# Kernel tuning notes

Hardware: AMD Instinct MI355X
Metric: run time of the kernel (lower is better)

Reference implementation:

```python
import jax, jax.numpy as jnp
import numpy as np

B, N, DE, H, DH = 2, 1024, 1024, 16, 64
DK = H * DH  # total complex qkv dim per stream
MIN_EXP = -30.0
EPS = 1e-4


def setup_inputs():
    key = jax.random.key(0)
    ks = jax.random.split(key, 8)

    def g(i, shape, sc=1.0):
        return jax.random.normal(ks[i], shape, jnp.float32) * sc

    # RoPE-style per-head frequencies for the conjugate-paired half-dims
    freqs = 10000.0 ** (-np.arange(DH // 2, dtype=np.float64) / (DH // 2))
    omega = jnp.asarray(np.tile(freqs[None, :], (H, 1)), jnp.float32)
    return {
        "x": g(0, (B, N, DE)),
        "Wq": g(1, (DE, 2 * DK), 1.0 / np.sqrt(DE)),
        "Wk": g(2, (DE, 2 * DK), 1.0 / np.sqrt(DE)),
        "Wv": g(3, (DE, 2 * DK), 1.0 / np.sqrt(DE)),
        "Wo": g(4, (2 * DK, DE), 1.0 / np.sqrt(2 * DK)),
        "omega": omega,
        "mu_raw": g(5, (H,)) - 2.0,          # pre-sigmoid decay rates
        "sigma_raw": g(6, (H,)),              # pre-softplus process noise
        "eta_raw": jnp.ones((H,), jnp.float32),
        "gamma_raw": jnp.ones((H,), jnp.float32),
        "tau": jnp.ones((H,), jnp.float32),   # inverse temperature
        "nu_raw": jnp.ones((H,), jnp.float32) * 4.0,  # robustness dof
    }


def reference(x, Wq, Wk, Wv, Wo, omega, mu_raw, sigma_raw, eta_raw, gamma_raw, tau, nu_raw):
    B_, N_, _ = x.shape
    H_, d_half = omega.shape
    DH_ = 2 * d_half
    DKt = H_ * DH_

    def cproj(W):
        z = x @ W                          # [B,N,2D] real/imag packed
        D = W.shape[1] // 2
        zc = jax.lax.complex(z[..., :D], z[..., D:])
        return zc.reshape(B_, N_, H_, DH_)

    q, k, v = cproj(Wq), cproj(Wk), cproj(Wv)

    # complex-conjugate-constrained rotations: omega stacked as [w, -w]
    om = jnp.concatenate([omega, -omega], axis=-1)              # [H,DH]
    t = jnp.arange(N_, dtype=jnp.float32)
    ang = t[:, None, None] * om[None]                           # [N,H,DH]
    phase = jax.lax.complex(jnp.cos(ang), jnp.sin(ang))
    qr = q * phase[None]
    kr = k * phase[None]

    # isotropic SDE decay kernel  E_rel = exp(-mu * |t_i - t_j|)
    mu = jax.nn.sigmoid(mu_raw) + EPS                           # [H]
    dt = jnp.abs(t[:, None] - t[None, :])                       # [N,N]
    E = jnp.exp(jnp.clip(-mu[:, None, None] * dt[None], MIN_EXP, 0.0))  # [H,N,N]

    # Re<q_i, Phi(dt) k_j>  (rotation carried by phases, decay by E)
    s = jnp.einsum('bihd,bjhd->bhij', qr, jnp.conj(kr)).real    # [B,H,N,N]
    qn = (q.real ** 2 + q.imag ** 2).sum(-1).transpose(0, 2, 1)  # [B,H,N]
    kn = (k.real ** 2 + k.imag ** 2).sum(-1).transpose(0, 2, 1)

    # Lyapunov-propagated uncertainty: P(dt) = sigma^2/(2mu)(1 - E^2) + eta^2 + gamma^2
    sigma_sq = jax.nn.softplus(sigma_raw)
    eta_sq = jax.nn.softplus(eta_raw)
    gamma_sq = jax.nn.softplus(gamma_raw)
    V = (sigma_sq / (2.0 * mu))[:, None, None] * (1.0 - E * E) \
        + (eta_sq + gamma_sq)[:, None, None]                    # [H,N,N]

    # per-head Mahalanobis residual under the SDE forecast
    maha = jnp.maximum(qn[..., None] + (E * E)[None] * kn[:, :, None, :]
                       - 2.0 * E[None] * s, 0.0) / V[None]      # [B,H,N,N]

    # robust nu-thresholding (Student-t style) + Gaussian normalization term
    nu = jax.nn.softplus(nu_raw)
    coef = (-0.5 * tau * (nu + DH_))[None, :, None, None]
    logits = coef * jnp.log1p(maha / nu[None, :, None, None]) \
             - 0.5 * DH_ * jnp.log(V)[None]

    causal = (t[:, None] >= t[None, :])
    logits = jnp.where(causal[None, None], logits, -jnp.inf)
    A = jax.nn.softmax(logits, axis=-1)                         # [B,H,N,N]

    out = jnp.einsum('bhij,bjhd->bihd', A.astype(v.dtype), v)   # complex [B,N,H,DH]
    y = jnp.concatenate([out.real.reshape(B_, N_, DKt),
                         out.imag.reshape(B_, N_, DKt)], axis=-1)
    return y @ Wo                                               # [B,N,DE]
```

## Files before the change

### kernel.cpp

```cpp
#include <hip/hip_runtime.h>
#include <math.h>

#define BB      2
#define NN      1024
#define DE_     1024
#define HH      16
#define TWO_DK  2048
#define PK      4194304
#define TBLR    1092

typedef float f32x4  __attribute__((ext_vector_type(4)));
typedef short bf16x8 __attribute__((ext_vector_type(8)));

__device__ __forceinline__ short f2bf(float f) {
    unsigned u = __float_as_uint(f);
    unsigned r = (u + 0x7fffu + ((u >> 16) & 1u)) >> 16;
    return (short)r;
}
__device__ __forceinline__ float bf2f(short v) {
    return __uint_as_float(((unsigned)(unsigned short)v) << 16);
}

__device__ __forceinline__ float fexp2(float x) { return __builtin_amdgcn_exp2f(x); }
__device__ __forceinline__ float flog2(float x) { return __builtin_amdgcn_logf(x); }

#define GLDS16(g, l) __builtin_amdgcn_global_load_lds(                        \
    (const __attribute__((address_space(1))) unsigned int*)(g),               \
    (__attribute__((address_space(3))) unsigned int*)(l), 16, 0, 0)
#define GLDS4(g, l) __builtin_amdgcn_global_load_lds(                         \
    (const __attribute__((address_space(1))) unsigned int*)(g),               \
    (__attribute__((address_space(3))) unsigned int*)(l), 4, 0, 0)

__constant__ int jIT[24] = {7,14,15,15, 6,12,13,13,14, 5,10,11,11,12,
                            4, 8, 9, 9,10, 3, 8, 2, 1, 0};
__constant__ int jJ0[24] = {0, 0, 0, 8, 0, 0, 0, 7, 8, 0, 0, 0, 6, 7,
                            0, 0, 0, 5, 6, 0, 5, 0, 0, 0};
__constant__ int jJ1[24] = {7, 7, 7,15, 6, 6, 6,13,14, 5, 5, 5,11,12,
                            4, 4, 4, 9,10, 3, 8, 2, 1, 0};
__constant__ int jPS[24] = {0, 1, 1, 2, 0, 1, 1, 2, 2, 0, 1, 1, 2, 2,
                            0, 1, 1, 2, 2, 0, 2, 0, 0, 0};

__global__ __launch_bounds__(256) void prep(
    const float* __restrict__ x,
    const float* __restrict__ Wq, const float* __restrict__ Wk,
    const float* __restrict__ Wv, const float* __restrict__ Wo,
    const float* __restrict__ mu_raw, const float* __restrict__ sigma_raw,
    const float* __restrict__ eta_raw, const float* __restrict__ gamma_raw,
    short* __restrict__ xb, short* __restrict__ wt, short* __restrict__ wot,
    float4* __restrict__ tbl) {
    const int z = blockIdx.z;
    if (z == 4) {
        const int flat = blockIdx.y * 32 + blockIdx.x;
        const int i = (flat * 256 + threadIdx.x) * 8;
        float4 v0 = *(const float4*)&x[i];
        float4 v1 = *(const float4*)&x[i + 4];
        short4 o0, o1;
        o0.x = f2bf(v0.x); o0.y = f2bf(v0.y); o0.z = f2bf(v0.z); o0.w = f2bf(v0.w);
        o1.x = f2bf(v1.x); o1.y = f2bf(v1.y); o1.z = f2bf(v1.z); o1.w = f2bf(v1.w);
        *(short4*)&xb[i] = o0; *(short4*)&xb[i + 4] = o1;
        return;
    }
    if (z == 3 && blockIdx.x >= 16) {
        const int idx = blockIdx.y * 16 + (blockIdx.x - 16);
        if (idx >= 80) return;
        const int h = idx / 5, rb = idx % 5;
        const int r = rb * 256 + threadIdx.x;
        if (r >= TBLR) return;
        const float mu = 1.f / (1.f + expf(-mu_raw[h])) + 1e-4f;
        const float Ac = log1pf(expf(sigma_raw[h])) / (2.f * mu);
        const float Cc = log1pf(expf(eta_raw[h])) + log1pf(expf(gamma_raw[h]));
        const float arg = fminf(fmaxf(-mu * (float)(r - 64), -30.f), 0.f);
        const float E   = expf(arg);
        const float V   = fmaf(Ac, 1.f - E * E, Cc);
        tbl[h * TBLR + r] = make_float4(2.f * E, 1.f / V, -32.f * log2f(V), E * E);
        return;
    }
    const float* in; short* out; int R, C;
    if (z < 3) { if (blockIdx.y >= 16) return;
                 in = (z == 0) ? Wq : (z == 1) ? Wk : Wv;
                 out = wt + (size_t)z * 2097152; R = 1024; C = 2048; }
    else       { in = Wo; out = wot; R = 2048; C = 1024; }
    __shared__ float t[64][65];
    const int c0 = blockIdx.x * 64, r0 = blockIdx.y * 64;
    const int tr = threadIdx.x >> 4, tc4 = (threadIdx.x & 15) * 4;
#pragma unroll
    for (int s = 0; s < 4; ++s) {
        const int r = tr + s * 16;
        float4 v = *(const float4*)&in[(size_t)(r0 + r) * C + c0 + tc4];
        t[r][tc4] = v.x; t[r][tc4 + 1] = v.y; t[r][tc4 + 2] = v.z; t[r][tc4 + 3] = v.w;
    }
    __syncthreads();
#pragma unroll
    for (int s = 0; s < 4; ++s) {
        const int oc = tr + s * 16;
        short4 o;
        o.x = f2bf(t[tc4 + 0][oc]); o.y = f2bf(t[tc4 + 1][oc]);
        o.z = f2bf(t[tc4 + 2][oc]); o.w = f2bf(t[tc4 + 3][oc]);
        *(short4*)&out[(size_t)(c0 + oc) * R + r0 + tc4] = o;
    }
}

__global__ __launch_bounds__(256, 5) void gemm_qkv_rot2(
    const short* __restrict__ A, const short* __restrict__ wt,
    const float* __restrict__ omega,
    short* __restrict__ qb, short* __restrict__ kb, short* __restrict__ vtb,
    float* __restrict__ qn_, float* __restrict__ kn_) {
    __shared__ __align__(16) short As[64 * 64];
    __shared__ __align__(16) short Bs[128 * 64];
    __shared__ float sN[4][64];
    const int tid = threadIdx.x;
    const int m0  = blockIdx.x * 64;
    const int h   = blockIdx.y;
    const short* W = wt + (size_t)blockIdx.z * 2097152;

    const short* aP[2]; int aOff[2];
#pragma unroll
    for (int i = 0; i < 2; ++i) {
        const int c   = i * 256 + tid;
        const int row = c >> 3;
        const int src = ((c & 7) ^ (row & 7)) << 3;
        aOff[i] = c * 8;
        aP[i] = A + (size_t)(m0 + row) * 1024 + src;
    }
    const short* bP[4]; int bOff[4];
#pragma unroll
    for (int i = 0; i < 4; ++i) {
        const int c   = i * 256 + tid;
        const int row = c >> 3;
        const int src = ((c & 7) ^ (row & 7)) << 3;
        bOff[i] = c * 8;
        const int t_ = row >> 5, u_ = (row >> 4) & 1, dcol = t_ * 16 + (row & 15);
        bP[i] = W + (size_t)(u_ * 1024 + h * 64 + dcol) * 1024 + src;
    }

    const int lane = tid & 63, w = tid >> 6;
    const int wc = w * 32;
    const int fr = lane & 15;
    const int fo = (lane >> 4) << 3;
    const int sw = (fr & 7) << 3;

    f32x4 acc[4][2];
#pragma unroll
    for (int a = 0; a < 4; ++a)
#pragma unroll
        for (int b = 0; b < 2; ++b) acc[a][b] = (f32x4){0.f, 0.f, 0.f, 0.f};

    for (int k0 = 0; k0 < 1024; k0 += 64) {
#pragma unroll
        for (int i = 0; i < 2; ++i) GLDS16(aP[i] + k0, &As[aOff[i]]);
#pragma unroll
        for (int i = 0; i < 4; ++i) GLDS16(bP[i] + k0, &Bs[bOff[i]]);
        __syncthreads();
#pragma unroll
        for (int ks = 0; ks < 64; ks += 32) {
            bf16x8 af[4], bf[2];
#pragma unroll
            for (int a = 0; a < 4; ++a)
                af[a] = *(const bf16x8*)&As[(a * 16 + fr) * 64 + ((ks + fo) ^ sw)];
#pragma unroll
            for (int b = 0; b < 2; ++b)
                bf[b] = *(const bf16x8*)&Bs[(wc + b * 16 + fr) * 64 + ((ks + fo) ^ sw)];
#pragma unroll
            for (int a = 0; a < 4; ++a)
#pragma unroll
                for (int b = 0; b < 2; ++b)
                    acc[a][b] = __builtin_amdgcn_mfma_f32_16x16x32_bf16(
                        af[a], bf[b], acc[a][b], 0, 0, 0);
        }
        __syncthreads();
    }

    const int quad = lane >> 4, cq = quad * 4, l15 = lane & 15;
    const int bh  = (m0 >> 10) * 16 + h;
    const int nb0 = (m0 & 1023) + cq;

    if (blockIdx.z == 2) {
#pragma unroll
        for (int a = 0; a < 4; ++a) {
#pragma unroll
            for (int b = 0; b < 2; ++b) {
                const int cl = wc + b * 16;
                const int dd = ((cl >> 4) & 1) * 64 + (cl >> 5) * 16 + l15;
                short4 o;
                o.x = f2bf(acc[a][b][0]); o.y = f2bf(acc[a][b][1]);
                o.z = f2bf(acc[a][b][2]); o.w = f2bf(acc[a][b][3]);
                *(short4*)&vtb[((size_t)bh * 128 + dd) * 1024 + nb0 + a * 16] = o;
            }
        }
        return;
    }
    float* nout = (blockIdx.z == 0) ? qn_ : kn_;
    short* obuf = (blockIdx.z == 0) ? qb  : kb;

#pragma unroll
    for (int a = 0; a < 4; ++a) {
        float ns[4] = {0.f, 0.f, 0.f, 0.f};
#pragma unroll
        for (int b = 0; b < 2; ++b)
#pragma unroll
            for (int r = 0; r < 4; ++r)
                ns[r] = fmaf(acc[a][b][r], acc[a][b][r], ns[r]);
#pragma unroll
        for (int m2 = 1; m2 < 16; m2 <<= 1)
#pragma unroll
            for (int r = 0; r < 4; ++r) ns[r] += __shfl_xor(ns[r], m2);
        if (l15 == 0)
#pragma unroll
            for (int r = 0; r < 4; ++r) sN[w][a * 16 + cq + r] = ns[r];
    }
    __syncthreads();
    if (tid < 64)
        nout[(size_t)bh * 1024 + (m0 & 1023) + tid] =
            sN[0][tid] + sN[1][tid] + sN[2][tid] + sN[3][tid];

    {
        const int d = w * 16 + l15;
        const float om = (d < 32) ? omega[h * 32 + d] : -omega[h * 32 + d - 32];
#pragma unroll
        for (int a = 0; a < 4; ++a) {
#pragma unroll
            for (int r = 0; r < 4; ++r) {
                const int n2 = nb0 + a * 16 + r;
                float sn, cs;
                __sincosf((float)n2 * om, &sn, &cs);
                const float re = acc[a][0][r], im = acc[a][1][r];
                short* orow = obuf + ((size_t)bh * 1024 + n2) * 128;
                orow[d]      = f2bf(re * cs - im * sn);
                orow[64 + d] = f2bf(re * sn + im * cs);
            }
        }
    }
}

__global__ __launch_bounds__(256) void attn_mfma(
    const short* __restrict__ qr, const short* __restrict__ kr,
    const short* __restrict__ vt,
    const float* __restrict__ qn, const float* __restrict__ kn,
    const float4* __restrict__ tbl,
    const float* __restrict__ tau_p, const float* __restrict__ nu_raw,
    short* __restrict__ y, short* __restrict__ po0, float* __restrict__ pml) {
    __shared__ __align__(16) short Ks[2][64 * 128];
    __shared__ __align__(16) short Vs[2][128 * 64];
    __shared__ __align__(16) short Ps[64 * 72];
    __shared__ __align__(16) float4 sT[2][128];
    __shared__ float sKn[2][64];

    const int bx   = blockIdx.x;
    const int xcd  = bx & 7;
    const int rest = bx >> 3;
    const int jrk  = rest >> 2;
    const int bh   = xcd * 4 + (rest & 3);
    const int h    = bh & 15;
    const int it   = jIT[jrk];
    const int j0j  = jJ0[jrk];
    const int j1j  = jJ1[jrk];
    const int psel = jPS[jrk];
    const int i0   = it * 64;
    const int pq   = bh * 8 + (it - 8);

    const int tid  = threadIdx.x;
    const int lane = tid & 63, w = tid >> 6;
    const int quad = lane >> 4, l15 = lane & 15;

    const float nu     = log1pf(expf(nu_raw[h]));
    const float coef   = -0.5f * tau_p[h] * (nu + 64.0f);
    const float inv_nu = 1.f / nu;

    const short* Qb  = qr + (size_t)bh * NN * 128;
    const short* Kb  = kr + (size_t)bh * NN * 128;
    const short* Vtb = vt + (size_t)bh * 128 * NN;

#define STAGE(JT, P) do {                                                     \
        const int j0_ = (JT) * 64, dt0_ = i0 - j0_;                           \
        _Pragma("unroll")                                                     \
        for (int i_ = 0; i_ < 4; ++i_) {                                      \
            const int c_ = i_ * 256 + tid, row_ = c_ >> 4;                    \
            const int src_ = ((c_ & 15) ^ (row_ & 7)) * 8;                    \
            GLDS16(Kb + (size_t)(j0_ + row_) * 128 + src_, &Ks[P][c_ * 8]);   \
        }                                                                     \
        _Pragma("unroll")                                                     \
        for (int i_ = 0; i_ < 4; ++i_) {                                      \
            const int c_ = i_ * 256 + tid, d_ = c_ >> 3;                      \
            const int src_ = ((c_ & 7) ^ (d_ & 7)) * 8;                       \
            GLDS16(Vtb + (size_t)d_ * NN + j0_ + src_, &Vs[P][c_ * 8]);       \
        }                                                                     \
        if (w == 0) {                                                         \
            GLDS16(tbl + h * TBLR + 1 + dt0_ + lane, &sT[P][lane]);           \
            GLDS16(tbl + h * TBLR + 65 + dt0_ + lane, &sT[P][64 + lane]);     \
        } else if (w == 1) {                                                  \
            GLDS4(kn + (size_t)bh * NN + j0_ + lane, &sKn[P][lane]);          \
        }                                                                     \
    } while (0)

    bf16x8 qf[4];
    const int arow = i0 + w * 16 + l15;
#pragma unroll
    for (int ks = 0; ks < 4; ++ks)
        qf[ks] = *(const bf16x8*)&Qb[(size_t)arow * 128 + ks * 32 + quad * 8];

    float mrow[4];
    f32x4 o[8];
    f32x4 o9 = (f32x4){0.f, 0.f, 0.f, 0.f};
#pragma unroll
    for (int r = 0; r < 4; ++r) mrow[r] = -INFINITY;
#pragma unroll
    for (int s = 0; s < 8; ++s) o[s] = (f32x4){0.f, 0.f, 0.f, 0.f};
    float qn4[4];
#pragma unroll
    for (int r = 0; r < 4; ++r)
        qn4[r] = qn[(size_t)bh * NN + i0 + w * 16 + quad * 4 + r];

    const bf16x8 onesv = (bf16x8){0x3F80, 0x3F80, 0x3F80, 0x3F80,
                                  0x3F80, 0x3F80, 0x3F80, 0x3F80};

    STAGE(j0j, 0);
    __syncthreads();

    for (int jt = j0j; jt <= j1j; ++jt) {
        const int p = (jt - j0j) & 1;
        if (jt < j1j) STAGE(jt + 1, 1 - p);

        f32x4 sAcc[4];
#pragma unroll
        for (int s = 0; s < 4; ++s) sAcc[s] = (f32x4){0.f, 0.f, 0.f, 0.f};
#pragma unroll
        for (int ks = 0; ks < 4; ++ks) {
#pragma unroll
            for (int s = 0; s < 4; ++s) {
                const int brow = s * 16 + l15;
                bf16x8 bK = *(const bf16x8*)&Ks[p][brow * 128 +
                                                  (((ks * 4 + quad) ^ (brow & 7)) * 8)];
                sAcc[s] = __builtin_amdgcn_mfma_f32_16x16x32_bf16(qf[ks], bK, sAcc[s], 0, 0, 0);
            }
        }

        float al[4];
        bool anyr = false;
#pragma unroll
        for (int r = 0; r < 4; ++r) {
            const int row = w * 16 + quad * 4 + r;
            float lg[4];
#pragma unroll
            for (int s = 0; s < 4; ++s) {
                const int col = s * 16 + l15;
                const float4 T = sT[p][row - col + 63];
                const float sv = sAcc[s][r];
                const float t1 = fmaf(T.w, sKn[p][col], qn4[r]);
                const float maha = fmaxf(fmaf(-T.x, sv, t1), 0.f) * T.y;
                float v = fmaf(coef, flog2(fmaf(maha, inv_nu, 1.f)), T.z);
                if (jt == it && col > row) v = -INFINITY;
                lg[s] = v;
            }
            float mx = fmaxf(fmaxf(lg[0], lg[1]), fmaxf(lg[2], lg[3]));
            mx = fmaxf(mx, __shfl_xor(mx, 1));
            mx = fmaxf(mx, __shfl_xor(mx, 2));
            mx = fmaxf(mx, __shfl_xor(mx, 4));
            mx = fmaxf(mx, __shfl_xor(mx, 8));
            const bool resc = mx > mrow[r] + 16.f;
            const float mu_ = resc ? mx : mrow[r];
            al[r] = resc ? fexp2(mrow[r] - mx) : 1.f;
            mrow[r] = mu_;
            anyr = anyr || resc;
#pragma unroll
            for (int s = 0; s < 4; ++s) {
                const float pv = fexp2(lg[s] - mu_);
                Ps[row * 72 + s * 16 + l15] = f2bf(pv);
            }
        }
        if (anyr) {
#pragma unroll
            for (int s = 0; s < 8; ++s)
#pragma unroll
                for (int r = 0; r < 4; ++r) o[s][r] *= al[r];
#pragma unroll
            for (int r = 0; r < 4; ++r) o9[r] *= al[r];
        }

#pragma unroll
        for (int jc = 0; jc < 2; ++jc) {
            bf16x8 aP = *(const bf16x8*)&Ps[(w * 16 + l15) * 72 + jc * 32 + quad * 8];
#pragma unroll
            for (int sub = 0; sub < 8; ++sub) {
                const int d = sub * 16 + l15;
                bf16x8 bV = *(const bf16x8*)&Vs[p][d * 64 + (((jc * 4 + quad) ^ (d & 7)) * 8)];
                o[sub] = __builtin_amdgcn_mfma_f32_16x16x32_bf16(aP, bV, o[sub], 0, 0, 0);
            }
            o9 = __builtin_amdgcn_mfma_f32_16x16x32_bf16(aP, onesv, o9, 0, 0, 0);
        }
        if (jt < j1j) __syncthreads();
    }
#undef STAGE

    short* dst = (psel == 1) ? po0 : y;
    const size_t rbase = (psel == 1) ? (size_t)pq * 64 : ((size_t)bh * NN + i0);
#pragma unroll
    for (int r = 0; r < 4; ++r) {
        const int lrow = w * 16 + quad * 4 + r;
        const float inv = 1.f / o9[r];
        const size_t base = (rbase + lrow) * 128;
#pragma unroll
        for (int sub = 0; sub < 8; ++sub)
            dst[base + sub * 16 + l15] = f2bf(o[sub][r] * inv);
        if (psel != 0 && l15 == 0)
            pml[(pq * 2 + (psel - 1)) * 64 + lrow] = mrow[r] + flog2(o9[r]);
    }
}

__global__ __launch_bounds__(256) void attn_merge(
    const short* __restrict__ po0, const float* __restrict__ pml,
    short* __restrict__ y) {
    const int qs = blockIdx.x;
    const int bh = qs >> 3, it = (qs & 7) + 8;
    const int t = threadIdx.x;
    const int row = t >> 2, dc = (t & 3) * 32;
    const float m1 = pml[(qs * 2 + 0) * 64 + row];
    const float m2 = pml[(qs * 2 + 1) * 64 + row];
    const float mx = fmaxf(m1, m2);
    const float w1 = fexp2(m1 - mx), w2 = fexp2(m2 - mx);
    const float inv = 1.f / (w1 + w2);
    const float a = w1 * inv, b = w2 * inv;
    const short* s1 = po0 + ((size_t)qs * 64 + row) * 128 + dc;
    short*       s2 = y + ((size_t)bh * NN + it * 64 + row) * 128 + dc;
#pragma unroll
    for (int i = 0; i < 32; i += 8) {
        bf16x8 v1 = *(const bf16x8*)(s1 + i);
        bf16x8 v2 = *(const bf16x8*)(s2 + i);
        bf16x8 ov;
#pragma unroll
        for (int k = 0; k < 8; ++k)
            ov[k] = f2bf(a * bf2f(v1[k]) + b * bf2f(v2[k]));
        *(bf16x8*)(s2 + i) = ov;
    }
}

__global__ __launch_bounds__(256) void gemm_out64(
    const short* __restrict__ yb, const short* __restrict__ wot,
    float* __restrict__ out) {
    __shared__ __align__(16) short As[2][64 * 64];
    __shared__ __align__(16) short Bs[2][64 * 64];
    const int tid = threadIdx.x;
    const int m0  = blockIdx.x * 64;
    const int n0  = blockIdx.y * 64;
    const int bb  = m0 >> 10;

    int aPre[2], aOff[2]; const short* bP[2];
#pragma unroll
    for (int i = 0; i < 2; ++i) {
        const int c = i * 256 + tid, row = c >> 3;
        const int src = ((c & 7) ^ (row & 7)) << 3;
        aPre[i] = ((m0 & 1023) + row) * 128 + src;
        bP[i] = wot + (size_t)(n0 + row) * 2048 + src;
        aOff[i] = c * 8;
    }

    const int lane = tid & 63, w = tid >> 6;
    const int wr = (w >> 1) * 32, wc = (w & 1) * 32;
    const int fr = lane & 15;
    const int fo = (lane >> 4) << 3;
    const int sw = (fr & 7) << 3;

    f32x4 acc[2][2];
#pragma unroll
    for (int a = 0; a < 2; ++a)
#pragma unroll
        for (int b = 0; b < 2; ++b) acc[a][b] = (f32x4){0.f, 0.f, 0.f, 0.f};

#define OSTAGE(KT, P) do {                                                    \
        const int k0_ = (KT) * 64;                                            \
        const int hh_ = (k0_ >> 6) & 15, im_ = k0_ >> 10;                     \
        const short* ab_ = yb + ((size_t)(bb * 16 + hh_) << 17) + im_ * 64;   \
        _Pragma("unroll")                                                     \
        for (int i_ = 0; i_ < 2; ++i_) GLDS16(ab_ + aPre[i_], &As[P][aOff[i_]]); \
        _Pragma("unroll")                                                     \
        for (int i_ = 0; i_ < 2; ++i_) GLDS16(bP[i_] + k0_, &Bs[P][aOff[i_]]);   \
    } while (0)

    OSTAGE(0, 0);
    __syncthreads();

    for (int kt = 0; kt < 32; ++kt) {
        const int p = kt & 1;
        if (kt < 31) OSTAGE(kt + 1, 1 - p);
#pragma unroll
        for (int ks = 0; ks < 64; ks += 32) {
            bf16x8 af[2], bf[2];
#pragma unroll
            for (int a = 0; a < 2; ++a)
                af[a] = *(const bf16x8*)&As[p][(wr + a * 16 + fr) * 64 + ((ks + fo) ^ sw)];
#pragma unroll
            for (int b = 0; b < 2; ++b)
                bf[b] = *(const bf16x8*)&Bs[p][(wc + b * 16 + fr) * 64 + ((ks + fo) ^ sw)];
#pragma unroll
            for (int a = 0; a < 2; ++a)
#pragma unroll
                for (int b = 0; b < 2; ++b)
                    acc[a][b] = __builtin_amdgcn_mfma_f32_16x16x32_bf16(
                        af[a], bf[b], acc[a][b], 0, 0, 0);
        }
        if (kt < 31) __syncthreads();
    }
#undef OSTAGE

    const int cq = (lane >> 4) * 4, l15 = lane & 15;
#pragma unroll
    for (int a = 0; a < 2; ++a)
#pragma unroll
        for (int b = 0; b < 2; ++b)
#pragma unroll
            for (int r = 0; r < 4; ++r)
                out[(size_t)(m0 + wr + a * 16 + cq + r) * 1024 +
                    (n0 + wc + b * 16 + l15)] = acc[a][b][r];
}

extern "C" void kernel_launch(void* const* d_in, const int* in_sizes, int n_in,
                              void* d_out, int out_size, void* d_ws, size_t ws_size,
                              hipStream_t stream) {
    const float* x         = (const float*)d_in[0];
    const float* Wq        = (const float*)d_in[1];
    const float* Wk        = (const float*)d_in[2];
    const float* Wv        = (const float*)d_in[3];
    const float* Wo        = (const float*)d_in[4];
    const float* omega     = (const float*)d_in[5];
    const float* mu_raw    = (const float*)d_in[6];
    const float* sigma_raw = (const float*)d_in[7];
    const float* eta_raw   = (const float*)d_in[8];
    const float* gamma_raw = (const float*)d_in[9];
    const float* tau       = (const float*)d_in[10];
    const float* nu_raw    = (const float*)d_in[11];
    float* out = (float*)d_out;

    short*  qb  = (short*)d_ws;
    short*  kb  = qb + PK;
    short*  vtb = kb + PK;
    float*  qn  = (float*)(vtb + PK);
    float*  kn  = qn + 32768;
    float4* tbl = (float4*)(kn + 32768);
    short*  wot = (short*)(tbl + HH * TBLR);
    short*  wt  = wot + 2097152;
    short*  xb  = wt + 3 * 2097152;
    short*  yb  = wt;
    short*  po0 = wt + 4194304;
    float*  pml = (float*)xb;

    prep<<<dim3(32, 32, 5), 256, 0, stream>>>(
        x, Wq, Wk, Wv, Wo, mu_raw, sigma_raw, eta_raw, gamma_raw,
        xb, wt, wot, tbl);
    gemm_qkv_rot2<<<dim3(32, 16, 3), 256, 0, stream>>>(
        xb, wt, omega, qb, kb, vtb, qn, kn);
    attn_mfma<<<dim3(768), 256, 0, stream>>>(
        qb, kb, vtb, qn, kn, tbl, tau, nu_raw, yb, po0, pml);
    attn_merge<<<dim3(256), 256, 0, stream>>>(po0, pml, yb);
    gemm_out64<<<dim3(32, 16), 256, 0, stream>>>(yb, wot, out);
}
```

Baseline: 200.0 us.

## Rebalance causal attention work into 512 blocks and load QKV weights directly to registers

The causal attention schedule changes from 768 blocks with 24 per-head work units to 512 blocks with 16 groups. Long query tiles are split into two halves that a merge kernel combines, and each short tile is paired with a longer one so the block runs both in turn. This aims for more even per-block work and fewer blocks, at the cost of an extra barrier and a longer serial loop per block. Separately, the QKV GEMM drops the B-matrix LDS staging and loads weight fragments straight from global memory into registers, lowering occupancy bounds from 5 to 4. This saves LDS traffic and space, but the uncoalesced direct global loads may cost more.

After: 217.1 us. 1.09x slower.

```diff
diff --git a/kernel.cpp b/kernel.cpp
--- a/kernel.cpp
+++ b/kernel.cpp
@@ -31,14 +31,11 @@
     (const __attribute__((address_space(1))) unsigned int*)(g),               \
     (__attribute__((address_space(3))) unsigned int*)(l), 4, 0, 0)
 
-__constant__ int jIT[24] = {7,14,15,15, 6,12,13,13,14, 5,10,11,11,12,
-                            4, 8, 9, 9,10, 3, 8, 2, 1, 0};
-__constant__ int jJ0[24] = {0, 0, 0, 8, 0, 0, 0, 7, 8, 0, 0, 0, 6, 7,
-                            0, 0, 0, 5, 6, 0, 5, 0, 0, 0};
-__constant__ int jJ1[24] = {7, 7, 7,15, 6, 6, 6,13,14, 5, 5, 5,11,12,
-                            4, 4, 4, 9,10, 3, 8, 2, 1, 0};
-__constant__ int jPS[24] = {0, 1, 1, 2, 0, 1, 1, 2, 2, 0, 1, 1, 2, 2,
-                            0, 1, 1, 2, 2, 0, 2, 0, 0, 0};
+__constant__ signed char gIT0[16] = {15,15,14,13,12,11,10, 9, 8, 7,14,13,12,11,10, 9};
+__constant__ signed char gJ00[16] = { 0, 8, 0, 0, 0, 0, 0, 0, 0, 0, 8, 8, 8, 8, 8, 8};
+__constant__ signed char gJ10[16] = { 7,15, 7, 7, 7, 7, 7, 7, 8, 7,14,13,12,11,10, 9};
+__constant__ signed char gPS0[16] = { 1, 2, 1, 1, 1, 1, 1, 1, 0, 0, 2, 2, 2, 2, 2, 2};
+__constant__ signed char gIT1[16] = {-1,-1,-1,-1,-1,-1,-1,-1,-1, 0, 1, 2, 3, 4, 5, 6};
 
 __global__ __launch_bounds__(256) void prep(
     const float* __restrict__ x,
@@ -100,13 +97,12 @@
     }
 }
 
-__global__ __launch_bounds__(256, 5) void gemm_qkv_rot2(
+__global__ __launch_bounds__(256, 4) void gemm_qkv_rot2(
     const short* __restrict__ A, const short* __restrict__ wt,
     const float* __restrict__ omega,
     short* __restrict__ qb, short* __restrict__ kb, short* __restrict__ vtb,
     float* __restrict__ qn_, float* __restrict__ kn_) {
     __shared__ __align__(16) short As[64 * 64];
-    __shared__ __align__(16) short Bs[128 * 64];
     __shared__ float sN[4][64];
     const int tid = threadIdx.x;
     const int m0  = blockIdx.x * 64;
@@ -122,23 +118,19 @@
         aOff[i] = c * 8;
         aP[i] = A + (size_t)(m0 + row) * 1024 + src;
     }
-    const short* bP[4]; int bOff[4];
-#pragma unroll
-    for (int i = 0; i < 4; ++i) {
-        const int c   = i * 256 + tid;
-        const int row = c >> 3;
-        const int src = ((c & 7) ^ (row & 7)) << 3;
-        bOff[i] = c * 8;
-        const int t_ = row >> 5, u_ = (row >> 4) & 1, dcol = t_ * 16 + (row & 15);
-        bP[i] = W + (size_t)(u_ * 1024 + h * 64 + dcol) * 1024 + src;
-    }
 
     const int lane = tid & 63, w = tid >> 6;
     const int wc = w * 32;
-    const int fr = lane & 15;
-    const int fo = (lane >> 4) << 3;
+    const int fr = lane & 15, quad = lane >> 4;
+    const int fo = quad << 3;
     const int sw = (fr & 7) << 3;
 
+    const int rB0 = wc + fr, rB1 = wc + 16 + fr;
+    const short* wB0 = W + (size_t)(((rB0 >> 4) & 1) * 1024 + h * 64 +
+                                    (rB0 >> 5) * 16 + (rB0 & 15)) * 1024 + fo;
+    const short* wB1 = W + (size_t)(((rB1 >> 4) & 1) * 1024 + h * 64 +
+                                    (rB1 >> 5) * 16 + (rB1 & 15)) * 1024 + fo;
+
     f32x4 acc[4][2];
 #pragma unroll
     for (int a = 0; a < 4; ++a)
@@ -148,29 +140,32 @@
     for (int k0 = 0; k0 < 1024; k0 += 64) {
 #pragma unroll
         for (int i = 0; i < 2; ++i) GLDS16(aP[i] + k0, &As[aOff[i]]);
-#pragma unroll
-        for (int i = 0; i < 4; ++i) GLDS16(bP[i] + k0, &Bs[bOff[i]]);
+        bf16x8 b00 = *(const bf16x8*)(wB0 + k0);
+        bf16x8 b01 = *(const bf16x8*)(wB0 + k0 + 32);
+        bf16x8 b10 = *(const bf16x8*)(wB1 + k0);
+        bf16x8 b11 = *(const bf16x8*)(wB1 + k0 + 32);
         __syncthreads();
-#pragma unroll
-        for (int ks = 0; ks < 64; ks += 32) {
-            bf16x8 af[4], bf[2];
-#pragma unroll
-            for (int a = 0; a < 4; ++a)
-                af[a] = *(const bf16x8*)&As[(a * 16 + fr) * 64 + ((ks + fo) ^ sw)];
-#pragma unroll
-            for (int b = 0; b < 2; ++b)
-                bf[b] = *(const bf16x8*)&Bs[(wc + b * 16 + fr) * 64 + ((ks + fo) ^ sw)];
-#pragma unroll
-            for (int a = 0; a < 4; ++a)
-#pragma unroll
-                for (int b = 0; b < 2; ++b)
-                    acc[a][b] = __builtin_amdgcn_mfma_f32_16x16x32_bf16(
-                        af[a], bf[b], acc[a][b], 0, 0, 0);
+        bf16x8 af0[4], af1[4];
+#pragma unroll
+        for (int a = 0; a < 4; ++a)
+            af0[a] = *(const bf16x8*)&As[(a * 16 + fr) * 64 + (fo ^ sw)];
+#pragma unroll
+        for (int a = 0; a < 4; ++a)
+            af1[a] = *(const bf16x8*)&As[(a * 16 + fr) * 64 + ((32 + fo) ^ sw)];
+#pragma unroll
+        for (int a = 0; a < 4; ++a) {
+            acc[a][0] = __builtin_amdgcn_mfma_f32_16x16x32_bf16(af0[a], b00, acc[a][0], 0, 0, 0);
+            acc[a][1] = __builtin_amdgcn_mfma_f32_16x16x32_bf16(af0[a], b10, acc[a][1], 0, 0, 0);
+        }
+#pragma unroll
+        for (int a = 0; a < 4; ++a) {
+            acc[a][0] = __builtin_amdgcn_mfma_f32_16x16x32_bf16(af1[a], b01, acc[a][0], 0, 0, 0);
+            acc[a][1] = __builtin_amdgcn_mfma_f32_16x16x32_bf16(af1[a], b11, acc[a][1], 0, 0, 0);
         }
         __syncthreads();
     }
 
-    const int quad = lane >> 4, cq = quad * 4, l15 = lane & 15;
+    const int cq = quad * 4, l15 = lane & 15;
     const int bh  = (m0 >> 10) * 16 + h;
     const int nb0 = (m0 & 1023) + cq;
 
@@ -248,15 +243,9 @@
     const int bx   = blockIdx.x;
     const int xcd  = bx & 7;
     const int rest = bx >> 3;
-    const int jrk  = rest >> 2;
     const int bh   = xcd * 4 + (rest & 3);
+    const int grp  = rest >> 2;
     const int h    = bh & 15;
-    const int it   = jIT[jrk];
-    const int j0j  = jJ0[jrk];
-    const int j1j  = jJ1[jrk];
-    const int psel = jPS[jrk];
-    const int i0   = it * 64;
-    const int pq   = bh * 8 + (it - 8);
 
     const int tid  = threadIdx.x;
     const int lane = tid & 63, w = tid >> 6;
@@ -269,6 +258,10 @@
     const short* Qb  = qr + (size_t)bh * NN * 128;
     const short* Kb  = kr + (size_t)bh * NN * 128;
     const short* Vtb = vt + (size_t)bh * 128 * NN;
+
+    const bf16x8 onesv = (bf16x8){0x3F80, 0x3F80, 0x3F80, 0x3F80,
+                                  0x3F80, 0x3F80, 0x3F80, 0x3F80};
+    const bool has2 = (gIT1[grp] >= 0);
 
 #define STAGE(JT, P) do {                                                     \
         const int j0_ = (JT) * 64, dt0_ = i0 - j0_;                           \
@@ -292,125 +285,135 @@
         }                                                                     \
     } while (0)
 
-    bf16x8 qf[4];
-    const int arow = i0 + w * 16 + l15;
-#pragma unroll
-    for (int ks = 0; ks < 4; ++ks)
-        qf[ks] = *(const bf16x8*)&Qb[(size_t)arow * 128 + ks * 32 + quad * 8];
-
-    float mrow[4];
-    f32x4 o[8];
-    f32x4 o9 = (f32x4){0.f, 0.f, 0.f, 0.f};
-#pragma unroll
-    for (int r = 0; r < 4; ++r) mrow[r] = -INFINITY;
-#pragma unroll
-    for (int s = 0; s < 8; ++s) o[s] = (f32x4){0.f, 0.f, 0.f, 0.f};
-    float qn4[4];
-#pragma unroll
-    for (int r = 0; r < 4; ++r)
-        qn4[r] = qn[(size_t)bh * NN + i0 + w * 16 + quad * 4 + r];
-
-    const bf16x8 onesv = (bf16x8){0x3F80, 0x3F80, 0x3F80, 0x3F80,
-                                  0x3F80, 0x3F80, 0x3F80, 0x3F80};
-
-    STAGE(j0j, 0);
-    __syncthreads();
-
-    for (int jt = j0j; jt <= j1j; ++jt) {
-        const int p = (jt - j0j) & 1;
-        if (jt < j1j) STAGE(jt + 1, 1 - p);
-
-        f32x4 sAcc[4];
-#pragma unroll
-        for (int s = 0; s < 4; ++s) sAcc[s] = (f32x4){0.f, 0.f, 0.f, 0.f};
-#pragma unroll
-        for (int ks = 0; ks < 4; ++ks) {
-#pragma unroll
-            for (int s = 0; s < 4; ++s) {
-                const int brow = s * 16 + l15;
-                bf16x8 bK = *(const bf16x8*)&Ks[p][brow * 128 +
-                                                  (((ks * 4 + quad) ^ (brow & 7)) * 8)];
-                sAcc[s] = __builtin_amdgcn_mfma_f32_16x16x32_bf16(qf[ks], bK, sAcc[s], 0, 0, 0);
+    for (int jj = 0; jj < 2; ++jj) {
+        int it, j0j, j1j, psel;
+        if (jj == 0) {
+            it = gIT0[grp]; j0j = gJ00[grp]; j1j = gJ10[grp]; psel = gPS0[grp];
+        } else {
+            if (!has2) break;
+            it = gIT1[grp]; j0j = 0; j1j = it; psel = 0;
+        }
+        const int i0 = it * 64;
+        const int pq = bh * 7 + (it - 9);
+
+        bf16x8 qf[4];
+        const int arow = i0 + w * 16 + l15;
+#pragma unroll
+        for (int ks = 0; ks < 4; ++ks)
+            qf[ks] = *(const bf16x8*)&Qb[(size_t)arow * 128 + ks * 32 + quad * 8];
+
+        float mrow[4];
+        f32x4 o[8];
+        f32x4 o9 = (f32x4){0.f, 0.f, 0.f, 0.f};
+#pragma unroll
+        for (int r = 0; r < 4; ++r) mrow[r] = -INFINITY;
+#pragma unroll
+        for (int s = 0; s < 8; ++s) o[s] = (f32x4){0.f, 0.f, 0.f, 0.f};
+        float qn4[4];
+#pragma unroll
+        for (int r = 0; r < 4; ++r)
+            qn4[r] = qn[(size_t)bh * NN + i0 + w * 16 + quad * 4 + r];
+
+        STAGE(j0j, 0);
+        __syncthreads();
+
+        for (int jt = j0j; jt <= j1j; ++jt) {
+            const int p = (jt - j0j) & 1;
+            if (jt < j1j) STAGE(jt + 1, 1 - p);
+
+            f32x4 sAcc[4];
+#pragma unroll
+            for (int s = 0; s < 4; ++s) sAcc[s] = (f32x4){0.f, 0.f, 0.f, 0.f};
+#pragma unroll
+            for (int ks = 0; ks < 4; ++ks) {
+#pragma unroll
+                for (int s = 0; s < 4; ++s) {
+                    const int brow = s * 16 + l15;
+                    bf16x8 bK = *(const bf16x8*)&Ks[p][brow * 128 +
+                                                      (((ks * 4 + quad) ^ (brow & 7)) * 8)];
+                    sAcc[s] = __builtin_amdgcn_mfma_f32_16x16x32_bf16(qf[ks], bK, sAcc[s], 0, 0, 0);
+                }
             }
-        }
-
-        float al[4];
-        bool anyr = false;
+
+            float al[4];
+            bool anyr = false;
+#pragma unroll
+            for (int r = 0; r < 4; ++r) {
+                const int row = w * 16 + quad * 4 + r;
+                float lg[4];
+#pragma unroll
+                for (int s = 0; s < 4; ++s) {
+                    const int col = s * 16 + l15;
+                    const float4 T = sT[p][row - col + 63];
+                    const float sv = sAcc[s][r];
+                    const float t1 = fmaf(T.w, sKn[p][col], qn4[r]);
+                    const float maha = fmaxf(fmaf(-T.x, sv, t1), 0.f) * T.y;
+                    float v = fmaf(coef, flog2(fmaf(maha, inv_nu, 1.f)), T.z);
+                    if (jt == it && col > row) v = -INFINITY;
+                    lg[s] = v;
+                }
+                float mx = fmaxf(fmaxf(lg[0], lg[1]), fmaxf(lg[2], lg[3]));
+                mx = fmaxf(mx, __shfl_xor(mx, 1));
+                mx = fmaxf(mx, __shfl_xor(mx, 2));
+                mx = fmaxf(mx, __shfl_xor(mx, 4));
+                mx = fmaxf(mx, __shfl_xor(mx, 8));
+                const bool resc = mx > mrow[r] + 16.f;
+                const float mu_ = resc ? mx : mrow[r];
+                al[r] = resc ? fexp2(mrow[r] - mx) : 1.f;
+                mrow[r] = mu_;
+                anyr = anyr || resc;
+#pragma unroll
+                for (int s = 0; s < 4; ++s) {
+                    const float pv = fexp2(lg[s] - mu_);
+                    Ps[row * 72 + s * 16 + l15] = f2bf(pv);
+                }
+            }
+            if (anyr) {
+#pragma unroll
+                for (int s = 0; s < 8; ++s)
+#pragma unroll
+                    for (int r = 0; r < 4; ++r) o[s][r] *= al[r];
+#pragma unroll
+                for (int r = 0; r < 4; ++r) o9[r] *= al[r];
+            }
+
+#pragma unroll
+            for (int jc = 0; jc < 2; ++jc) {
+                bf16x8 aP = *(const bf16x8*)&Ps[(w * 16 + l15) * 72 + jc * 32 + quad * 8];
+#pragma unroll
+                for (int sub = 0; sub < 8; ++sub) {
+                    const int d = sub * 16 + l15;
+                    bf16x8 bV = *(const bf16x8*)&Vs[p][d * 64 + (((jc * 4 + quad) ^ (d & 7)) * 8)];
+                    o[sub] = __builtin_amdgcn_mfma_f32_16x16x32_bf16(aP, bV, o[sub], 0, 0, 0);
+                }
+                o9 = __builtin_amdgcn_mfma_f32_16x16x32_bf16(aP, onesv, o9, 0, 0, 0);
+            }
+            if (jt < j1j) __syncthreads();
+        }
+
+        short* dst = (psel == 1) ? po0 : y;
+        const size_t rbase = (psel == 1) ? (size_t)pq * 64 : ((size_t)bh * NN + i0);
 #pragma unroll
         for (int r = 0; r < 4; ++r) {
-            const int row = w * 16 + quad * 4 + r;
-            float lg[4];
-#pragma unroll
-            for (int s = 0; s < 4; ++s) {
-                const int col = s * 16 + l15;
-                const float4 T = sT[p][row - col + 63];
-                const float sv = sAcc[s][r];
-                const float t1 = fmaf(T.w, sKn[p][col], qn4[r]);
-                const float maha = fmaxf(fmaf(-T.x, sv, t1), 0.f) * T.y;
-                float v = fmaf(coef, flog2(fmaf(maha, inv_nu, 1.f)), T.z);
-                if (jt == it && col > row) v = -INFINITY;
-                lg[s] = v;
-            }
-            float mx = fmaxf(fmaxf(lg[0], lg[1]), fmaxf(lg[2], lg[3]));
-            mx = fmaxf(mx, __shfl_xor(mx, 1));
-            mx = fmaxf(mx, __shfl_xor(mx, 2));
-            mx = fmaxf(mx, __shfl_xor(mx, 4));
-            mx = fmaxf(mx, __shfl_xor(mx, 8));
-            const bool resc = mx > mrow[r] + 16.f;
-            const float mu_ = resc ? mx : mrow[r];
-            al[r] = resc ? fexp2(mrow[r] - mx) : 1.f;
-            mrow[r] = mu_;
-            anyr = anyr || resc;
-#pragma unroll
-            for (int s = 0; s < 4; ++s) {
-                const float pv = fexp2(lg[s] - mu_);
-                Ps[row * 72 + s * 16 + l15] = f2bf(pv);
-            }
-        }
-        if (anyr) {
-#pragma unroll
-            for (int s = 0; s < 8; ++s)
-#pragma unroll
-                for (int r = 0; r < 4; ++r) o[s][r] *= al[r];
-#pragma unroll
-            for (int r = 0; r < 4; ++r) o9[r] *= al[r];
-        }
-
-#pragma unroll
-        for (int jc = 0; jc < 2; ++jc) {
-            bf16x8 aP = *(const bf16x8*)&Ps[(w * 16 + l15) * 72 + jc * 32 + quad * 8];
-#pragma unroll
-            for (int sub = 0; sub < 8; ++sub) {
-                const int d = sub * 16 + l15;
-                bf16x8 bV = *(const bf16x8*)&Vs[p][d * 64 + (((jc * 4 + quad) ^ (d & 7)) * 8)];
-                o[sub] = __builtin_amdgcn_mfma_f32_16x16x32_bf16(aP, bV, o[sub], 0, 0, 0);
-            }
-            o9 = __builtin_amdgcn_mfma_f32_16x16x32_bf16(aP, onesv, o9, 0, 0, 0);
-        }
-        if (jt < j1j) __syncthreads();
+            const int lrow = w * 16 + quad * 4 + r;
+            const float inv = 1.f / o9[r];
+            const size_t base = (rbase + lrow) * 128;
+#pragma unroll
+            for (int sub = 0; sub < 8; ++sub)
+                dst[base + sub * 16 + l15] = f2bf(o[sub][r] * inv);
+            if (psel != 0 && l15 == 0)
+                pml[(pq * 2 + (psel - 1)) * 64 + lrow] = mrow[r] + flog2(o9[r]);
+        }
+        if (jj == 0 && has2) __syncthreads();
     }
 #undef STAGE
-
-    short* dst = (psel == 1) ? po0 : y;
-    const size_t rbase = (psel == 1) ? (size_t)pq * 64 : ((size_t)bh * NN + i0);
-#pragma unroll
-    for (int r = 0; r < 4; ++r) {
-        const int lrow = w * 16 + quad * 4 + r;
-        const float inv = 1.f / o9[r];
-        const size_t base = (rbase + lrow) * 128;
-#pragma unroll
-        for (int sub = 0; sub < 8; ++sub)
-            dst[base + sub * 16 + l15] = f2bf(o[sub][r] * inv);
-        if (psel != 0 && l15 == 0)
-            pml[(pq * 2 + (psel - 1)) * 64 + lrow] = mrow[r] + flog2(o9[r]);
-    }
 }
 
 __global__ __launch_bounds__(256) void attn_merge(
     const short* __restrict__ po0, const float* __restrict__ pml,
     short* __restrict__ y) {
     const int qs = blockIdx.x;
-    const int bh = qs >> 3, it = (qs & 7) + 8;
+    const int bh = qs / 7, it = qs % 7 + 9;
     const int t = threadIdx.x;
     const int row = t >> 2, dc = (t & 3) * 32;
     const float m1 = pml[(qs * 2 + 0) * 64 + row];
@@ -547,8 +550,8 @@
         xb, wt, wot, tbl);
     gemm_qkv_rot2<<<dim3(32, 16, 3), 256, 0, stream>>>(
         xb, wt, omega, qb, kb, vtb, qn, kn);
-    attn_mfma<<<dim3(768), 256, 0, stream>>>(
+    attn_mfma<<<dim3(512), 256, 0, stream>>>(
         qb, kb, vtb, qn, kn, tbl, tau, nu_raw, yb, po0, pml);
-    attn_merge<<<dim3(256), 256, 0, stream>>>(po0, pml, yb);
+    attn_merge<<<dim3(224), 256, 0, stream>>>(po0, pml, yb);
     gemm_out64<<<dim3(32, 16), 256, 0, stream>>>(yb, wot, out);
 }
```

## Rebalance causal attention work into 16 groups per head with paired query tiles

Applied to the files above, without the earlier changes.

Replaces the 24-entry per-(b,h) work table with a 16-group schedule. Some blocks now process two query tiles in sequence, pairing a long split tile with a short one, so 512 blocks cover the causal triangle with more even per-block work. Only tiles 9-15 are split, so the merge kernel shrinks to 224 blocks. In exchange, each block runs a serial second pass with an extra barrier.

Result: no change. 201.2 us (+0.6%).

```diff
diff --git a/kernel.cpp b/kernel.cpp
--- a/kernel.cpp
+++ b/kernel.cpp
@@ -31,14 +31,11 @@
     (const __attribute__((address_space(1))) unsigned int*)(g),               \
     (__attribute__((address_space(3))) unsigned int*)(l), 4, 0, 0)
 
-__constant__ int jIT[24] = {7,14,15,15, 6,12,13,13,14, 5,10,11,11,12,
-                            4, 8, 9, 9,10, 3, 8, 2, 1, 0};
-__constant__ int jJ0[24] = {0, 0, 0, 8, 0, 0, 0, 7, 8, 0, 0, 0, 6, 7,
-                            0, 0, 0, 5, 6, 0, 5, 0, 0, 0};
-__constant__ int jJ1[24] = {7, 7, 7,15, 6, 6, 6,13,14, 5, 5, 5,11,12,
-                            4, 4, 4, 9,10, 3, 8, 2, 1, 0};
-__constant__ int jPS[24] = {0, 1, 1, 2, 0, 1, 1, 2, 2, 0, 1, 1, 2, 2,
-                            0, 1, 1, 2, 2, 0, 2, 0, 0, 0};
+__constant__ signed char gIT0[16] = {15,15,14,13,12,11,10, 9, 8, 7,14,13,12,11,10, 9};
+__constant__ signed char gJ00[16] = { 0, 8, 0, 0, 0, 0, 0, 0, 0, 0, 8, 8, 8, 8, 8, 8};
+__constant__ signed char gJ10[16] = { 7,15, 7, 7, 7, 7, 7, 7, 8, 7,14,13,12,11,10, 9};
+__constant__ signed char gPS0[16] = { 1, 2, 1, 1, 1, 1, 1, 1, 0, 0, 2, 2, 2, 2, 2, 2};
+__constant__ signed char gIT1[16] = {-1,-1,-1,-1,-1,-1,-1,-1,-1, 0, 1, 2, 3, 4, 5, 6};
 
 __global__ __launch_bounds__(256) void prep(
     const float* __restrict__ x,
@@ -248,15 +245,9 @@
     const int bx   = blockIdx.x;
     const int xcd  = bx & 7;
     const int rest = bx >> 3;
-    const int jrk  = rest >> 2;
     const int bh   = xcd * 4 + (rest & 3);
+    const int grp  = rest >> 2;
     const int h    = bh & 15;
-    const int it   = jIT[jrk];
-    const int j0j  = jJ0[jrk];
-    const int j1j  = jJ1[jrk];
-    const int psel = jPS[jrk];
-    const int i0   = it * 64;
-    const int pq   = bh * 8 + (it - 8);
 
     const int tid  = threadIdx.x;
     const int lane = tid & 63, w = tid >> 6;
@@ -269,6 +260,10 @@
     const short* Qb  = qr + (size_t)bh * NN * 128;
     const short* Kb  = kr + (size_t)bh * NN * 128;
     const short* Vtb = vt + (size_t)bh * 128 * NN;
+
+    const bf16x8 onesv = (bf16x8){0x3F80, 0x3F80, 0x3F80, 0x3F80,
+                                  0x3F80, 0x3F80, 0x3F80, 0x3F80};
+    const bool has2 = (gIT1[grp] >= 0);
 
 #define STAGE(JT, P) do {                                                     \
         const int j0_ = (JT) * 64, dt0_ = i0 - j0_;                           \
@@ -292,125 +287,135 @@
         }                                                                     \
     } while (0)
 
-    bf16x8 qf[4];
-    const int arow = i0 + w * 16 + l15;
-#pragma unroll
-    for (int ks = 0; ks < 4; ++ks)
-        qf[ks] = *(const bf16x8*)&Qb[(size_t)arow * 128 + ks * 32 + quad * 8];
-
-    float mrow[4];
-    f32x4 o[8];
-    f32x4 o9 = (f32x4){0.f, 0.f, 0.f, 0.f};
-#pragma unroll
-    for (int r = 0; r < 4; ++r) mrow[r] = -INFINITY;
-#pragma unroll
-    for (int s = 0; s < 8; ++s) o[s] = (f32x4){0.f, 0.f, 0.f, 0.f};
-    float qn4[4];
-#pragma unroll
-    for (int r = 0; r < 4; ++r)
-        qn4[r] = qn[(size_t)bh * NN + i0 + w * 16 + quad * 4 + r];
-
-    const bf16x8 onesv = (bf16x8){0x3F80, 0x3F80, 0x3F80, 0x3F80,
-                                  0x3F80, 0x3F80, 0x3F80, 0x3F80};
-
-    STAGE(j0j, 0);
-    __syncthreads();
-
-    for (int jt = j0j; jt <= j1j; ++jt) {
-        const int p = (jt - j0j) & 1;
-        if (jt < j1j) STAGE(jt + 1, 1 - p);
-
-        f32x4 sAcc[4];
-#pragma unroll
-        for (int s = 0; s < 4; ++s) sAcc[s] = (f32x4){0.f, 0.f, 0.f, 0.f};
-#pragma unroll
-        for (int ks = 0; ks < 4; ++ks) {
-#pragma unroll
-            for (int s = 0; s < 4; ++s) {
-                const int brow = s * 16 + l15;
-                bf16x8 bK = *(const bf16x8*)&Ks[p][brow * 128 +
-                                                  (((ks * 4 + quad) ^ (brow & 7)) * 8)];
-                sAcc[s] = __builtin_amdgcn_mfma_f32_16x16x32_bf16(qf[ks], bK, sAcc[s], 0, 0, 0);
+    for (int jj = 0; jj < 2; ++jj) {
+        int it, j0j, j1j, psel;
+        if (jj == 0) {
+            it = gIT0[grp]; j0j = gJ00[grp]; j1j = gJ10[grp]; psel = gPS0[grp];
+        } else {
+            if (!has2) break;
+            it = gIT1[grp]; j0j = 0; j1j = it; psel = 0;
+        }
+        const int i0 = it * 64;
+        const int pq = bh * 7 + (it - 9);
+
+        bf16x8 qf[4];
+        const int arow = i0 + w * 16 + l15;
+#pragma unroll
+        for (int ks = 0; ks < 4; ++ks)
+            qf[ks] = *(const bf16x8*)&Qb[(size_t)arow * 128 + ks * 32 + quad * 8];
+
+        float mrow[4];
+        f32x4 o[8];
+        f32x4 o9 = (f32x4){0.f, 0.f, 0.f, 0.f};
+#pragma unroll
+        for (int r = 0; r < 4; ++r) mrow[r] = -INFINITY;
+#pragma unroll
+        for (int s = 0; s < 8; ++s) o[s] = (f32x4){0.f, 0.f, 0.f, 0.f};
+        float qn4[4];
+#pragma unroll
+        for (int r = 0; r < 4; ++r)
+            qn4[r] = qn[(size_t)bh * NN + i0 + w * 16 + quad * 4 + r];
+
+        STAGE(j0j, 0);
+        __syncthreads();
+
+        for (int jt = j0j; jt <= j1j; ++jt) {
+            const int p = (jt - j0j) & 1;
+            if (jt < j1j) STAGE(jt + 1, 1 - p);
+
+            f32x4 sAcc[4];
+#pragma unroll
+            for (int s = 0; s < 4; ++s) sAcc[s] = (f32x4){0.f, 0.f, 0.f, 0.f};
+#pragma unroll
+            for (int ks = 0; ks < 4; ++ks) {
+#pragma unroll
+                for (int s = 0; s < 4; ++s) {
+                    const int brow = s * 16 + l15;
+                    bf16x8 bK = *(const bf16x8*)&Ks[p][brow * 128 +
+                                                      (((ks * 4 + quad) ^ (brow & 7)) * 8)];
+                    sAcc[s] = __builtin_amdgcn_mfma_f32_16x16x32_bf16(qf[ks], bK, sAcc[s], 0, 0, 0);
+                }
             }
-        }
-
-        float al[4];
-        bool anyr = false;
+
+            float al[4];
+            bool anyr = false;
+#pragma unroll
+            for (int r = 0; r < 4; ++r) {
+                const int row = w * 16 + quad * 4 + r;
+                float lg[4];
+#pragma unroll
+                for (int s = 0; s < 4; ++s) {
+                    const int col = s * 16 + l15;
+                    const float4 T = sT[p][row - col + 63];
+                    const float sv = sAcc[s][r];
+                    const float t1 = fmaf(T.w, sKn[p][col], qn4[r]);
+                    const float maha = fmaxf(fmaf(-T.x, sv, t1), 0.f) * T.y;
+                    float v = fmaf(coef, flog2(fmaf(maha, inv_nu, 1.f)), T.z);
+                    if (jt == it && col > row) v = -INFINITY;
+                    lg[s] = v;
+                }
+                float mx = fmaxf(fmaxf(lg[0], lg[1]), fmaxf(lg[2], lg[3]));
+                mx = fmaxf(mx, __shfl_xor(mx, 1));
+                mx = fmaxf(mx, __shfl_xor(mx, 2));
+                mx = fmaxf(mx, __shfl_xor(mx, 4));
+                mx = fmaxf(mx, __shfl_xor(mx, 8));
+                const bool resc = mx > mrow[r] + 16.f;
+                const float mu_ = resc ? mx : mrow[r];
+                al[r] = resc ? fexp2(mrow[r] - mx) : 1.f;
+                mrow[r] = mu_;
+                anyr = anyr || resc;
+#pragma unroll
+                for (int s = 0; s < 4; ++s) {
+                    const float pv = fexp2(lg[s] - mu_);
+                    Ps[row * 72 + s * 16 + l15] = f2bf(pv);
+                }
+            }
+            if (anyr) {
+#pragma unroll
+                for (int s = 0; s < 8; ++s)
+#pragma unroll
+                    for (int r = 0; r < 4; ++r) o[s][r] *= al[r];
+#pragma unroll
+                for (int r = 0; r < 4; ++r) o9[r] *= al[r];
+            }
+
+#pragma unroll
+            for (int jc = 0; jc < 2; ++jc) {
+                bf16x8 aP = *(const bf16x8*)&Ps[(w * 16 + l15) * 72 + jc * 32 + quad * 8];
+#pragma unroll
+                for (int sub = 0; sub < 8; ++sub) {
+                    const int d = sub * 16 + l15;
+                    bf16x8 bV = *(const bf16x8*)&Vs[p][d * 64 + (((jc * 4 + quad) ^ (d & 7)) * 8)];
+                    o[sub] = __builtin_amdgcn_mfma_f32_16x16x32_bf16(aP, bV, o[sub], 0, 0, 0);
+                }
+                o9 = __builtin_amdgcn_mfma_f32_16x16x32_bf16(aP, onesv, o9, 0, 0, 0);
+            }
+            if (jt < j1j) __syncthreads();
+        }
+
+        short* dst = (psel == 1) ? po0 : y;
+        const size_t rbase = (psel == 1) ? (size_t)pq * 64 : ((size_t)bh * NN + i0);
 #pragma unroll
         for (int r = 0; r < 4; ++r) {
-            const int row = w * 16 + quad * 4 + r;
-            float lg[4];
-#pragma unroll
-            for (int s = 0; s < 4; ++s) {
-                const int col = s * 16 + l15;
-                const float4 T = sT[p][row - col + 63];
-                const float sv = sAcc[s][r];
-                const float t1 = fmaf(T.w, sKn[p][col], qn4[r]);
-                const float maha = fmaxf(fmaf(-T.x, sv, t1), 0.f) * T.y;
-                float v = fmaf(coef, flog2(fmaf(maha, inv_nu, 1.f)), T.z);
-                if (jt == it && col > row) v = -INFINITY;
-                lg[s] = v;
-            }
-            float mx = fmaxf(fmaxf(lg[0], lg[1]), fmaxf(lg[2], lg[3]));
-            mx = fmaxf(mx, __shfl_xor(mx, 1));
-            mx = fmaxf(mx, __shfl_xor(mx, 2));
-            mx = fmaxf(mx, __shfl_xor(mx, 4));
-            mx = fmaxf(mx, __shfl_xor(mx, 8));
-            const bool resc = mx > mrow[r] + 16.f;
-            const float mu_ = resc ? mx : mrow[r];
-            al[r] = resc ? fexp2(mrow[r] - mx) : 1.f;
-            mrow[r] = mu_;
-            anyr = anyr || resc;
-#pragma unroll
-            for (int s = 0; s < 4; ++s) {
-                const float pv = fexp2(lg[s] - mu_);
-                Ps[row * 72 + s * 16 + l15] = f2bf(pv);
-            }
-        }
-        if (anyr) {
-#pragma unroll
-            for (int s = 0; s < 8; ++s)
-#pragma unroll
-                for (int r = 0; r < 4; ++r) o[s][r] *= al[r];
-#pragma unroll
-            for (int r = 0; r < 4; ++r) o9[r] *= al[r];
-        }
-
-#pragma unroll
-        for (int jc = 0; jc < 2; ++jc) {
-            bf16x8 aP = *(const bf16x8*)&Ps[(w * 16 + l15) * 72 + jc * 32 + quad * 8];
-#pragma unroll
-            for (int sub = 0; sub < 8; ++sub) {
-                const int d = sub * 16 + l15;
-                bf16x8 bV = *(const bf16x8*)&Vs[p][d * 64 + (((jc * 4 + quad) ^ (d & 7)) * 8)];
-                o[sub] = __builtin_amdgcn_mfma_f32_16x16x32_bf16(aP, bV, o[sub], 0, 0, 0);
-            }
-            o9 = __builtin_amdgcn_mfma_f32_16x16x32_bf16(aP, onesv, o9, 0, 0, 0);
-        }
-        if (jt < j1j) __syncthreads();
+            const int lrow = w * 16 + quad * 4 + r;
+            const float inv = 1.f / o9[r];
+            const size_t base = (rbase + lrow) * 128;
+#pragma unroll
+            for (int sub = 0; sub < 8; ++sub)
+                dst[base + sub * 16 + l15] = f2bf(o[sub][r] * inv);
+            if (psel != 0 && l15 == 0)
+                pml[(pq * 2 + (psel - 1)) * 64 + lrow] = mrow[r] + flog2(o9[r]);
+        }
+        if (jj == 0 && has2) __syncthreads();
     }
 #undef STAGE
-
-    short* dst = (psel == 1) ? po0 : y;
-    const size_t rbase = (psel == 1) ? (size_t)pq * 64 : ((size_t)bh * NN + i0);
-#pragma unroll
-    for (int r = 0; r < 4; ++r) {
-        const int lrow = w * 16 + quad * 4 + r;
-        const float inv = 1.f / o9[r];
-        const size_t base = (rbase + lrow) * 128;
-#pragma unroll
-        for (int sub = 0; sub < 8; ++sub)
-            dst[base + sub * 16 + l15] = f2bf(o[sub][r] * inv);
-        if (psel != 0 && l15 == 0)
-            pml[(pq * 2 + (psel - 1)) * 64 + lrow] = mrow[r] + flog2(o9[r]);
-    }
 }
 
 __global__ __launch_bounds__(256) void attn_merge(
     const short* __restrict__ po0, const float* __restrict__ pml,
     short* __restrict__ y) {
     const int qs = blockIdx.x;
-    const int bh = qs >> 3, it = (qs & 7) + 8;
+    const int bh = qs / 7, it = qs % 7 + 9;
     const int t = threadIdx.x;
     const int row = t >> 2, dc = (t & 3) * 32;
     const float m1 = pml[(qs * 2 + 0) * 64 + row];
@@ -547,8 +552,8 @@
         xb, wt, wot, tbl);
     gemm_qkv_rot2<<<dim3(32, 16, 3), 256, 0, stream>>>(
         xb, wt, omega, qb, kb, vtb, qn, kn);
-    attn_mfma<<<dim3(768), 256, 0, stream>>>(
+    attn_mfma<<<dim3(512), 256, 0, stream>>>(
         qb, kb, vtb, qn, kn, tbl, tau, nu_raw, yb, po0, pml);
-    attn_merge<<<dim3(256), 256, 0, stream>>>(po0, pml, yb);
+    attn_merge<<<dim3(224), 256, 0, stream>>>(po0, pml, yb);
     gemm_out64<<<dim3(32, 16), 256, 0, stream>>>(yb, wot, out);
 }
```
